# Optimization experiments

Measured on AMD Instinct MI355X. Metric: run time of the kernel, lower is better.

## Reference

```python
import jax, jax.numpy as jnp
import numpy as np

N_NODES = 50000
N_EDGES = 800000
D = 64
N_BASIS = 8


def setup_inputs() -> dict:
    key = jax.random.key(0)
    ks = jax.random.split(key, 16)
    inp = {
        "p": jax.random.normal(ks[0], (N_NODES, D), dtype=jnp.float32),
        "idx_i": jax.random.randint(ks[1], (N_EDGES,), 0, N_NODES),
        "idx_j": jax.random.randint(ks[2], (N_EDGES,), 0, N_NODES),
        "basis": jax.random.normal(ks[3], (N_EDGES, N_BASIS), dtype=jnp.float32),
        # pp_layer MLP: [64, 64, 64], activation tanh between layers
        "pp_W1": jax.random.normal(ks[4], (D, D), dtype=jnp.float32) / np.sqrt(D),
        "pp_b1": jnp.zeros((D,), dtype=jnp.float32),
        "pp_W2": jax.random.normal(ks[5], (D, D), dtype=jnp.float32) / np.sqrt(D),
        "pp_b2": jnp.zeros((D,), dtype=jnp.float32),
        # pi_layer MLP: n_neurons = [128, 64, 64, 64*8], activation=None, last layer no bias
        "pi_W1": jax.random.normal(ks[6], (2 * D, D), dtype=jnp.float32) / np.sqrt(2 * D),
        "pi_b1": jnp.zeros((D,), dtype=jnp.float32),
        "pi_W2": jax.random.normal(ks[7], (D, D), dtype=jnp.float32) / np.sqrt(D),
        "pi_b2": jnp.zeros((D,), dtype=jnp.float32),
        "pi_W3": jax.random.normal(ks[8], (D, D * N_BASIS), dtype=jnp.float32) / np.sqrt(D),
        # ii_layer MLP: [64, 64, 64], activation tanh between layers
        "ii_W1": jax.random.normal(ks[9], (D, D), dtype=jnp.float32) / np.sqrt(D),
        "ii_b1": jnp.zeros((D,), dtype=jnp.float32),
        "ii_W2": jax.random.normal(ks[10], (D, D), dtype=jnp.float32) / np.sqrt(D),
        "ii_b2": jnp.zeros((D,), dtype=jnp.float32),
    }
    return inp


def reference(p, idx_i, idx_j, basis,
              pp_W1, pp_b1, pp_W2, pp_b2,
              pi_W1, pi_b1, pi_W2, pi_b2, pi_W3,
              ii_W1, ii_b1, ii_W2, ii_b2):
    # pp_layer: node MLP (tanh between layers, no activation after last)
    p1 = jnp.tanh(p @ pp_W1 + pp_b1) @ pp_W2 + pp_b2          # [N, D]

    # PILayer: gather endpoint features, concat, linear MLP (activation=None), basis contraction
    inter = jnp.concatenate([p1[idx_i], p1[idx_j]], axis=-1)  # [E, 2D]
    inter = inter @ pi_W1 + pi_b1                              # [E, D]
    inter = inter @ pi_W2 + pi_b2                              # [E, D]
    inter = inter @ pi_W3                                      # [E, D*n_basis] (no bias)
    inter = inter.reshape(inter.shape[0], D, N_BASIS)          # [E, D, n_basis]
    i1 = jnp.einsum('ecb,eb->ec', inter, basis)                # [E, D]

    # ii_layer: edge MLP
    i1 = jnp.tanh(i1 @ ii_W1 + ii_b1) @ ii_W2 + ii_b2          # [E, D]

    # IPLayer: scatter_add edge features back to nodes (dim_size = p1.shape[0])
    out = jax.ops.segment_sum(i1, idx_j, num_segments=p1.shape[0])  # [N, D]
    return out
```

## Files before the change

### kernel.cpp

```cpp
#include <hip/hip_runtime.h>

#define N_NODES 50000
#define N_EDGES 800000
#define NPAD 50176

typedef float f32x4 __attribute__((ext_vector_type(4)));
typedef short bf16x8 __attribute__((ext_vector_type(8)));

__device__ __forceinline__ float fast_tanh(float x) {
  float e = __expf(2.0f * x);
  float r;
  asm("v_rcp_f32 %0, %1" : "=v"(r) : "v"(e + 1.0f));
  return fmaf(-2.0f, r, 1.0f);
}

__device__ __forceinline__ unsigned short f2bf_rne(float x) {
  unsigned u = __float_as_uint(x);
  unsigned r = u + 0x7FFFu + ((u >> 16) & 1u);
  return (unsigned short)(r >> 16);
}

__device__ __forceinline__ void gemm8(const float* __restrict__ sXrow,
                                      const float* __restrict__ sW,
                                      int lane, float acc[8]) {
  for (int k = 0; k < 64; k += 4) {
    float w0 = sW[k * 64 + lane];
    float w1 = sW[(k + 1) * 64 + lane];
    float w2 = sW[(k + 2) * 64 + lane];
    float w3 = sW[(k + 3) * 64 + lane];
    #pragma unroll
    for (int r = 0; r < 8; ++r) {
      float4 x = *(const float4*)(sXrow + r * 64 + k);
      acc[r] = fmaf(x.x, w0, fmaf(x.y, w1, fmaf(x.z, w2, fmaf(x.w, w3, acc[r]))));
    }
  }
}

__global__ __launch_bounds__(256) void front_kernel(
    const float* __restrict__ p, const int* __restrict__ idx_j,
    const float* __restrict__ ppW1, const float* __restrict__ ppb1,
    const float* __restrict__ ppW2, const float* __restrict__ ppb2,
    const float* __restrict__ piW1, const float* __restrict__ pib1,
    const float* __restrict__ piW2, const float* __restrict__ pib2,
    const float* __restrict__ piW3, const float* __restrict__ iiW1,
    const float* __restrict__ iiW2,
    int* __restrict__ counts,
    float* __restrict__ qa, float* __restrict__ qb, float* __restrict__ b12,
    unsigned short* __restrict__ Bpack, unsigned short* __restrict__ W2pack) {
  int bid = blockIdx.x;
  int tid = threadIdx.x;

  if (bid >= 1708) {
    int e = (bid - 1708) * 256 + tid;
    if (e < N_EDGES) atomicAdd(&counts[idx_j[e]], 1);
    return;
  }
  if (bid >= 1563) {
    int gid = (bid - 1563) * 256 + tid;
    if (gid < 32768) {
      int j = gid & 7;
      int lane = (gid >> 3) & 63;
      int ct = (gid >> 9) & 3;
      int ks = gid >> 11;
      int kidx = ks * 32 + ((lane >> 4) << 3) + j;
      int col = ct * 16 + (lane & 15);
      int k = kidx >> 3, b = kidx & 7;
      float acc = 0.f;
      #pragma unroll 8
      for (int mm = 0; mm < 64; ++mm)
        acc = fmaf(piW3[k * 512 + mm * 8 + b], iiW1[mm * 64 + col], acc);
      Bpack[gid] = f2bf_rne(acc);
    } else if (gid < 32832) {
      int c = gid - 32768;
      float acc = pib2[c];
      for (int k = 0; k < 64; ++k) acc = fmaf(pib1[k], piW2[k * 64 + c], acc);
      b12[c] = acc;
    } else if (gid < 36928) {
      int g2 = gid - 32832;
      int j = g2 & 7;
      int lane = (g2 >> 3) & 63;
      int ct = (g2 >> 9) & 3;
      int ks = g2 >> 11;
      int kidx = ks * 32 + ((lane >> 4) << 3) + j;
      int col = ct * 16 + (lane & 15);
      W2pack[g2] = f2bf_rne(iiW2[kidx * 64 + col]);
    }
    return;
  }

  __shared__ float sW[64 * 64];
  __shared__ float sX[4][8][64];
  __shared__ float sY[4][8][64];
  int wave = tid >> 6, lane = tid & 63;
  int rowbase = bid * 32 + wave * 8;

  float4* sXf4 = (float4*)&sX[wave][0][0];
  for (int t = lane; t < 128; t += 64) {
    int r = t >> 4, c4 = t & 15;
    int row = rowbase + r;
    float4 v = make_float4(0.f, 0.f, 0.f, 0.f);
    if (row < N_NODES) v = ((const float4*)p)[row * 16 + c4];
    sXf4[t] = v;
  }
  for (int i = tid; i < 4096; i += 256) sW[i] = ppW1[i];
  __syncthreads();
  float h[8];
  {
    float bv = ppb1[lane];
    #pragma unroll
    for (int r = 0; r < 8; ++r) h[r] = bv;
  }
  gemm8(&sX[wave][0][0], sW, lane, h);
  #pragma unroll
  for (int r = 0; r < 8; ++r) sY[wave][r][lane] = fast_tanh(h[r]);
  __syncthreads();
  for (int i = tid; i < 4096; i += 256) sW[i] = ppW2[i];
  __syncthreads();
  float g[8];
  {
    float bv = ppb2[lane];
    #pragma unroll
    for (int r = 0; r < 8; ++r) g[r] = bv;
  }
  gemm8(&sY[wave][0][0], sW, lane, g);
  #pragma unroll
  for (int r = 0; r < 8; ++r) sX[wave][r][lane] = g[r];
  __syncthreads();
  for (int i = tid; i < 4096; i += 256) sW[i] = piW1[i];
  __syncthreads();
  float t1[8] = {0, 0, 0, 0, 0, 0, 0, 0};
  gemm8(&sX[wave][0][0], sW, lane, t1);
  #pragma unroll
  for (int r = 0; r < 8; ++r) sY[wave][r][lane] = t1[r];
  __syncthreads();
  for (int i = tid; i < 4096; i += 256) sW[i] = piW1[4096 + i];
  __syncthreads();
  float t2[8] = {0, 0, 0, 0, 0, 0, 0, 0};
  gemm8(&sX[wave][0][0], sW, lane, t2);
  __syncthreads();
  #pragma unroll
  for (int r = 0; r < 8; ++r) sX[wave][r][lane] = t2[r];
  __syncthreads();
  for (int i = tid; i < 4096; i += 256) sW[i] = piW2[i];
  __syncthreads();
  float a[8] = {0, 0, 0, 0, 0, 0, 0, 0};
  float b[8] = {0, 0, 0, 0, 0, 0, 0, 0};
  for (int k = 0; k < 64; k += 4) {
    float w0 = sW[k * 64 + lane];
    float w1 = sW[(k + 1) * 64 + lane];
    float w2 = sW[(k + 2) * 64 + lane];
    float w3 = sW[(k + 3) * 64 + lane];
    #pragma unroll
    for (int r = 0; r < 8; ++r) {
      float4 x = *(const float4*)(&sY[wave][r][k]);
      float4 y = *(const float4*)(&sX[wave][r][k]);
      a[r] = fmaf(x.x, w0, fmaf(x.y, w1, fmaf(x.z, w2, fmaf(x.w, w3, a[r]))));
      b[r] = fmaf(y.x, w0, fmaf(y.y, w1, fmaf(y.z, w2, fmaf(y.w, w3, b[r]))));
    }
  }
  #pragma unroll
  for (int r = 0; r < 8; ++r) {
    int row = rowbase + r;
    if (row < N_NODES) {
      qa[row * 64 + lane] = a[r];
      qb[row * 64 + lane] = b[r];
    }
  }
}

__global__ __launch_bounds__(1024) void scan_kernel(
    const int* __restrict__ counts, int* __restrict__ cursors) {
  __shared__ int buf[1024];
  __shared__ int red[16];
  int b = blockIdx.x, tid = threadIdx.x;
  int idx = b * 1024 + tid;
  int v = counts[idx];
  buf[tid] = v;
  int partial = 0;
  for (int i = tid; i < b * 1024; i += 1024) partial += counts[i];
  #pragma unroll
  for (int off = 32; off >= 1; off >>= 1) partial += __shfl_down(partial, off, 64);
  if ((tid & 63) == 0) red[tid >> 6] = partial;
  __syncthreads();
  for (int off = 1; off < 1024; off <<= 1) {
    int t = (tid >= off) ? buf[tid - off] : 0;
    __syncthreads();
    buf[tid] += t;
    __syncthreads();
  }
  int base = 0;
  #pragma unroll
  for (int i = 0; i < 16; ++i) base += red[i];
  cursors[idx] = base + buf[tid] - v;
}

__global__ __launch_bounds__(256) void sort_scatter_kernel(
    const int* __restrict__ idx_i, const int* __restrict__ idx_j,
    int* __restrict__ cursors,
    int2* __restrict__ sorted_ij, int* __restrict__ sorted_e) {
  int e = blockIdx.x * 256 + threadIdx.x;
  if (e < N_EDGES) {
    int j = idx_j[e];
    int pos = atomicAdd(&cursors[j], 1);
    sorted_ij[pos] = make_int2(idx_i[e], j);
    sorted_e[pos] = e;
  }
}

__global__ __launch_bounds__(1024, 8) void edge_kernel(
    const int2* __restrict__ sorted_ij, const int* __restrict__ sorted_e,
    const float* __restrict__ basis,
    const float* __restrict__ qa, const float* __restrict__ qb,
    const float* __restrict__ b12,
    const unsigned short* __restrict__ Bpack,
    const unsigned short* __restrict__ W2pack,
    const float* __restrict__ iib1, const float* __restrict__ iib2,
    float* __restrict__ out) {
  __shared__ __align__(16) unsigned short sB[32768];
  float* sH2 = (float*)sB;
  unsigned short* sT = sB;
  float* sF = (float*)sB;

  int tid = threadIdx.x;
  int e0 = blockIdx.x * 256;

  for (int t = tid; t < 4096; t += 1024) {
    int e = t >> 4, q = t & 15;
    int2 se = sorted_ij[e0 + e];
    float4 va = ((const float4*)qa)[se.x * 16 + q];
    float4 vb = ((const float4*)qb)[se.y * 16 + q];
    float4 vc = ((const float4*)b12)[q];
    float4 h;
    h.x = va.x + vb.x + vc.x;
    h.y = va.y + vb.y + vc.y;
    h.z = va.z + vb.z + vc.z;
    h.w = va.w + vb.w + vc.w;
    int dw = e * 64 + ((q * 4) ^ ((e & 7) << 3));
    *((float4*)(sH2 + dw)) = h;
  }
  __syncthreads();

  int w = tid >> 6, l = tid & 63;
  int m = l & 15, s = l >> 4;
  int eloc = w * 16 + m;
  int swz = (eloc & 7) << 3;

  float h2r[16];
  #pragma unroll
  for (int t = 0; t < 16; ++t) h2r[t] = sH2[eloc * 64 + ((t * 4 + s) ^ swz)];

  float bas[8];
  {
    int eorig = sorted_e[e0 + eloc];
    const float4* bp = (const float4*)(basis + (size_t)eorig * 8);
    float4 b0 = bp[0], b1 = bp[1];
    bas[0] = b0.x; bas[1] = b0.y; bas[2] = b0.z; bas[3] = b0.w;
    bas[4] = b1.x; bas[5] = b1.y; bas[6] = b1.z; bas[7] = b1.w;
  }
  __syncthreads();

  {
    const uint4* g = (const uint4*)Bpack;
    uint4* d = (uint4*)sB;
    #pragma unroll
    for (int t = 0; t < 4; ++t) d[tid + t * 1024] = g[tid + t * 1024];
  }
  __syncthreads();

  f32x4 c0, c1, c2, c3;
  {
    float v0 = iib1[m], v1 = iib1[16 + m], v2 = iib1[32 + m], v3 = iib1[48 + m];
    c0 = (f32x4){v0, v0, v0, v0};
    c1 = (f32x4){v1, v1, v1, v1};
    c2 = (f32x4){v2, v2, v2, v2};
    c3 = (f32x4){v3, v3, v3, v3};
  }

  const bf16x8* Bl = (const bf16x8*)sB;
  #pragma unroll
  for (int ks = 0; ks < 16; ++ks) {
    bf16x8 B0 = Bl[(ks * 4 + 0) * 64 + l];
    bf16x8 B1 = Bl[(ks * 4 + 1) * 64 + l];
    bf16x8 B2 = Bl[(ks * 4 + 2) * 64 + l];
    bf16x8 B3 = Bl[(ks * 4 + 3) * 64 + l];
    float hv = h2r[ks];
    union { unsigned u[4]; bf16x8 v; } A;
    #pragma unroll
    for (int j = 0; j < 4; ++j) {
      float p0 = hv * bas[2 * j];
      float p1 = hv * bas[2 * j + 1];
      asm("v_cvt_pk_bf16_f32 %0, %1, %2" : "=v"(A.u[j]) : "v"(p0), "v"(p1));
    }
    c0 = __builtin_amdgcn_mfma_f32_16x16x32_bf16(A.v, B0, c0, 0, 0, 0);
    c1 = __builtin_amdgcn_mfma_f32_16x16x32_bf16(A.v, B1, c1, 0, 0, 0);
    c2 = __builtin_amdgcn_mfma_f32_16x16x32_bf16(A.v, B2, c2, 0, 0, 0);
    c3 = __builtin_amdgcn_mfma_f32_16x16x32_bf16(A.v, B3, c3, 0, 0, 0);
  }
  __syncthreads();

  #pragma unroll
  for (int r = 0; r < 4; ++r) {
    int row = w * 16 + s * 4 + r;
    sT[row * 72 + 0 * 16 + m] = f2bf_rne(fast_tanh(c0[r]));
    sT[row * 72 + 1 * 16 + m] = f2bf_rne(fast_tanh(c1[r]));
    sT[row * 72 + 2 * 16 + m] = f2bf_rne(fast_tanh(c2[r]));
    sT[row * 72 + 3 * 16 + m] = f2bf_rne(fast_tanh(c3[r]));
  }
  __syncthreads();

  f32x4 d0, d1, d2, d3;
  {
    float v0 = iib2[m], v1 = iib2[16 + m], v2 = iib2[32 + m], v3 = iib2[48 + m];
    d0 = (f32x4){v0, v0, v0, v0};
    d1 = (f32x4){v1, v1, v1, v1};
    d2 = (f32x4){v2, v2, v2, v2};
    d3 = (f32x4){v3, v3, v3, v3};
  }
  const bf16x8* Wl = (const bf16x8*)W2pack;
  #pragma unroll
  for (int ks = 0; ks < 2; ++ks) {
    bf16x8 Af = *(const bf16x8*)(sT + eloc * 72 + ks * 32 + s * 8);
    d0 = __builtin_amdgcn_mfma_f32_16x16x32_bf16(Af, Wl[(ks * 4 + 0) * 64 + l], d0, 0, 0, 0);
    d1 = __builtin_amdgcn_mfma_f32_16x16x32_bf16(Af, Wl[(ks * 4 + 1) * 64 + l], d1, 0, 0, 0);
    d2 = __builtin_amdgcn_mfma_f32_16x16x32_bf16(Af, Wl[(ks * 4 + 2) * 64 + l], d2, 0, 0, 0);
    d3 = __builtin_amdgcn_mfma_f32_16x16x32_bf16(Af, Wl[(ks * 4 + 3) * 64 + l], d3, 0, 0, 0);
  }

  #pragma unroll
  for (int h = 0; h < 2; ++h) {
    __syncthreads();
    if ((w >> 3) == h) {
      int wl = w & 7;
      #pragma unroll
      for (int r = 0; r < 4; ++r) {
        int row = wl * 16 + s * 4 + r;
        sF[row * 68 + 0  + m] = d0[r];
        sF[row * 68 + 16 + m] = d1[r];
        sF[row * 68 + 32 + m] = d2[r];
        sF[row * 68 + 48 + m] = d3[r];
      }
    }
    __syncthreads();
    {
      int base_e = e0 + h * 128 + w * 8;
      float acc = sF[(w * 8) * 68 + l];
      int cur_j = sorted_ij[base_e].y;
      #pragma unroll
      for (int rr = 1; rr < 8; ++rr) {
        int nj = sorted_ij[base_e + rr].y;
        float v = sF[(w * 8 + rr) * 68 + l];
        if (nj == cur_j) {
          acc += v;
        } else {
          atomicAdd(&out[(size_t)cur_j * 64 + l], acc);
          acc = v;
          cur_j = nj;
        }
      }
      atomicAdd(&out[(size_t)cur_j * 64 + l], acc);
    }
  }
}

extern "C" void kernel_launch(void* const* d_in, const int* in_sizes, int n_in,
                              void* d_out, int out_size, void* d_ws, size_t ws_size,
                              hipStream_t stream) {
  const float* p     = (const float*)d_in[0];
  const int*   idx_i = (const int*)d_in[1];
  const int*   idx_j = (const int*)d_in[2];
  const float* basis = (const float*)d_in[3];
  const float* ppW1  = (const float*)d_in[4];
  const float* ppb1  = (const float*)d_in[5];
  const float* ppW2  = (const float*)d_in[6];
  const float* ppb2  = (const float*)d_in[7];
  const float* piW1  = (const float*)d_in[8];
  const float* pib1  = (const float*)d_in[9];
  const float* piW2  = (const float*)d_in[10];
  const float* pib2  = (const float*)d_in[11];
  const float* piW3  = (const float*)d_in[12];
  const float* iiW1  = (const float*)d_in[13];
  const float* iib1  = (const float*)d_in[14];
  const float* iiW2  = (const float*)d_in[15];
  const float* iib2  = (const float*)d_in[16];

  float* ws  = (float*)d_ws;
  float* qa  = ws;
  float* qb  = ws + 3200000;
  float* b12 = ws + 6400000;
  unsigned short* Bpack  = (unsigned short*)(ws + 6400064);
  unsigned short* W2pack = (unsigned short*)(ws + 6416448);
  int* counts    = (int*)(ws + 6418496);
  int* cursors   = (int*)(ws + 6468672);
  int2* sorted_ij = (int2*)(ws + 6518848);
  int* sorted_e   = (int*)(ws + 8118848);

  hipMemsetAsync(d_out, 0, (size_t)out_size * sizeof(float), stream);
  hipMemsetAsync(counts, 0, (size_t)NPAD * sizeof(int), stream);
  front_kernel<<<4833, 256, 0, stream>>>(p, idx_j, ppW1, ppb1, ppW2, ppb2,
                                         piW1, pib1, piW2, pib2, piW3, iiW1, iiW2,
                                         counts, qa, qb, b12, Bpack, W2pack);
  scan_kernel<<<49, 1024, 0, stream>>>(counts, cursors);
  sort_scatter_kernel<<<3125, 256, 0, stream>>>(idx_i, idx_j, cursors,
                                                sorted_ij, sorted_e);
  edge_kernel<<<3125, 1024, 0, stream>>>(sorted_ij, sorted_e, basis,
                                         qa, qb, b12, Bpack, W2pack,
                                         iib1, iib2, (float*)d_out);
}
```

Measured before the change: 300.6 us.

## Move node-side MLP chain in front kernel to bf16 MFMA with swizzled LDS

Rewrites the front kernel's node MLP chain (pp layers plus the pi_W1/pi_W2 projections) to use 16x16x32 bf16 MFMA instructions in place of scalar fp32 FMAs. Activations and weights are packed to bf16 in XOR-swizzled shared memory to avoid bank conflicts. Each block now handles 128 node rows with 512 threads, so the grid split for the counting and packing roles is rescaled. Intermediates are rounded to bf16, which costs accuracy in qa/qb, but this kernel is only one part of the total time.

```diff
diff --git a/kernel.cpp b/kernel.cpp
--- a/kernel.cpp
+++ b/kernel.cpp
@@ -20,23 +20,56 @@
   return (unsigned short)(r >> 16);
 }
 
-__device__ __forceinline__ void gemm8(const float* __restrict__ sXrow,
-                                      const float* __restrict__ sW,
-                                      int lane, float acc[8]) {
-  for (int k = 0; k < 64; k += 4) {
-    float w0 = sW[k * 64 + lane];
-    float w1 = sW[(k + 1) * 64 + lane];
-    float w2 = sW[(k + 2) * 64 + lane];
-    float w3 = sW[(k + 3) * 64 + lane];
-    #pragma unroll
-    for (int r = 0; r < 8; ++r) {
-      float4 x = *(const float4*)(sXrow + r * 64 + k);
-      acc[r] = fmaf(x.x, w0, fmaf(x.y, w1, fmaf(x.z, w2, fmaf(x.w, w3, acc[r]))));
-    }
-  }
-}
-
-__global__ __launch_bounds__(256) void front_kernel(
+__device__ __forceinline__ void packW(const float* __restrict__ W,
+                                      unsigned short* __restrict__ dst, int tid) {
+  int ks = tid >> 8, ct = (tid >> 6) & 3, lane = tid & 63;
+  int k0 = ks * 32 + ((lane >> 4) << 3);
+  int col = ct * 16 + (lane & 15);
+  const float* src = W + k0 * 64 + col;
+  unsigned u[4];
+  #pragma unroll
+  for (int jj = 0; jj < 4; ++jj) {
+    float v0 = src[(2 * jj) * 64];
+    float v1 = src[(2 * jj + 1) * 64];
+    asm("v_cvt_pk_bf16_f32 %0, %1, %2" : "=v"(u[jj]) : "v"(v0), "v"(v1));
+  }
+  *(uint4*)(dst + (size_t)tid * 8) = make_uint4(u[0], u[1], u[2], u[3]);
+}
+
+__device__ __forceinline__ void mfma_gemm(const unsigned short* __restrict__ actIn,
+                                          const unsigned short* __restrict__ bpk,
+                                          int w, int l, f32x4 acc[4]) {
+  int m = l & 15, s = l >> 4;
+  int row = w * 16 + m;
+  int sw = (m & 7) << 3;
+  #pragma unroll
+  for (int ks = 0; ks < 2; ++ks) {
+    bf16x8 a = *(const bf16x8*)(actIn + row * 64 + ((ks * 32 + s * 8) ^ sw));
+    #pragma unroll
+    for (int ct = 0; ct < 4; ++ct) {
+      bf16x8 b = *(const bf16x8*)(bpk + ((size_t)((ks * 4 + ct) * 64 + l)) * 8);
+      acc[ct] = __builtin_amdgcn_mfma_f32_16x16x32_bf16(a, b, acc[ct], 0, 0, 0);
+    }
+  }
+}
+
+__device__ __forceinline__ void store_act(unsigned short* __restrict__ actOut,
+                                          int w, int l, const f32x4 acc[4],
+                                          bool do_tanh) {
+  int m = l & 15, s = l >> 4;
+  #pragma unroll
+  for (int ct = 0; ct < 4; ++ct) {
+    #pragma unroll
+    for (int r = 0; r < 4; ++r) {
+      int row = w * 16 + s * 4 + r;
+      float v = acc[ct][r];
+      if (do_tanh) v = fast_tanh(v);
+      actOut[row * 64 + ((ct * 16 + m) ^ ((row & 7) << 3))] = f2bf_rne(v);
+    }
+  }
+}
+
+__global__ __launch_bounds__(512) void front_kernel(
     const float* __restrict__ p, const int* __restrict__ idx_j,
     const float* __restrict__ ppW1, const float* __restrict__ ppb1,
     const float* __restrict__ ppW2, const float* __restrict__ ppb2,
@@ -50,13 +83,13 @@
   int bid = blockIdx.x;
   int tid = threadIdx.x;
 
-  if (bid >= 1708) {
-    int e = (bid - 1708) * 256 + tid;
+  if (bid >= 464) {
+    int e = (bid - 464) * 512 + tid;
     if (e < N_EDGES) atomicAdd(&counts[idx_j[e]], 1);
     return;
   }
-  if (bid >= 1563) {
-    int gid = (bid - 1563) * 256 + tid;
+  if (bid >= 391) {
+    int gid = (bid - 391) * 512 + tid;
     if (gid < 32768) {
       int j = gid & 7;
       int lane = (gid >> 3) & 63;
@@ -88,83 +121,91 @@
     return;
   }
 
-  __shared__ float sW[64 * 64];
-  __shared__ float sX[4][8][64];
-  __shared__ float sY[4][8][64];
-  int wave = tid >> 6, lane = tid & 63;
-  int rowbase = bid * 32 + wave * 8;
-
-  float4* sXf4 = (float4*)&sX[wave][0][0];
-  for (int t = lane; t < 128; t += 64) {
-    int r = t >> 4, c4 = t & 15;
-    int row = rowbase + r;
+  __shared__ __align__(16) unsigned short sBpk[2][4096];
+  __shared__ __align__(16) unsigned short sAct[2][8192];
+
+  int w = tid >> 6, l = tid & 63;
+  int m = l & 15;
+  int nb0 = bid * 128;
+
+  for (int t = tid; t < 2048; t += 512) {
+    int row = t >> 4, q = t & 15;
+    int g = nb0 + row;
     float4 v = make_float4(0.f, 0.f, 0.f, 0.f);
-    if (row < N_NODES) v = ((const float4*)p)[row * 16 + c4];
-    sXf4[t] = v;
-  }
-  for (int i = tid; i < 4096; i += 256) sW[i] = ppW1[i];
-  __syncthreads();
-  float h[8];
-  {
-    float bv = ppb1[lane];
-    #pragma unroll
-    for (int r = 0; r < 8; ++r) h[r] = bv;
-  }
-  gemm8(&sX[wave][0][0], sW, lane, h);
-  #pragma unroll
-  for (int r = 0; r < 8; ++r) sY[wave][r][lane] = fast_tanh(h[r]);
-  __syncthreads();
-  for (int i = tid; i < 4096; i += 256) sW[i] = ppW2[i];
-  __syncthreads();
-  float g[8];
-  {
-    float bv = ppb2[lane];
-    #pragma unroll
-    for (int r = 0; r < 8; ++r) g[r] = bv;
-  }
-  gemm8(&sY[wave][0][0], sW, lane, g);
-  #pragma unroll
-  for (int r = 0; r < 8; ++r) sX[wave][r][lane] = g[r];
-  __syncthreads();
-  for (int i = tid; i < 4096; i += 256) sW[i] = piW1[i];
-  __syncthreads();
-  float t1[8] = {0, 0, 0, 0, 0, 0, 0, 0};
-  gemm8(&sX[wave][0][0], sW, lane, t1);
-  #pragma unroll
-  for (int r = 0; r < 8; ++r) sY[wave][r][lane] = t1[r];
-  __syncthreads();
-  for (int i = tid; i < 4096; i += 256) sW[i] = piW1[4096 + i];
-  __syncthreads();
-  float t2[8] = {0, 0, 0, 0, 0, 0, 0, 0};
-  gemm8(&sX[wave][0][0], sW, lane, t2);
-  __syncthreads();
-  #pragma unroll
-  for (int r = 0; r < 8; ++r) sX[wave][r][lane] = t2[r];
-  __syncthreads();
-  for (int i = tid; i < 4096; i += 256) sW[i] = piW2[i];
-  __syncthreads();
-  float a[8] = {0, 0, 0, 0, 0, 0, 0, 0};
-  float b[8] = {0, 0, 0, 0, 0, 0, 0, 0};
-  for (int k = 0; k < 64; k += 4) {
-    float w0 = sW[k * 64 + lane];
-    float w1 = sW[(k + 1) * 64 + lane];
-    float w2 = sW[(k + 2) * 64 + lane];
-    float w3 = sW[(k + 3) * 64 + lane];
-    #pragma unroll
-    for (int r = 0; r < 8; ++r) {
-      float4 x = *(const float4*)(&sY[wave][r][k]);
-      float4 y = *(const float4*)(&sX[wave][r][k]);
-      a[r] = fmaf(x.x, w0, fmaf(x.y, w1, fmaf(x.z, w2, fmaf(x.w, w3, a[r]))));
-      b[r] = fmaf(y.x, w0, fmaf(y.y, w1, fmaf(y.z, w2, fmaf(y.w, w3, b[r]))));
-    }
-  }
-  #pragma unroll
-  for (int r = 0; r < 8; ++r) {
-    int row = rowbase + r;
-    if (row < N_NODES) {
-      qa[row * 64 + lane] = a[r];
-      qb[row * 64 + lane] = b[r];
-    }
+    if (g < N_NODES) v = ((const float4*)p)[g * 16 + q];
+    unsigned u0, u1;
+    asm("v_cvt_pk_bf16_f32 %0, %1, %2" : "=v"(u0) : "v"(v.x), "v"(v.y));
+    asm("v_cvt_pk_bf16_f32 %0, %1, %2" : "=v"(u1) : "v"(v.z), "v"(v.w));
+    int sw = (row & 7) << 3;
+    *(uint2*)(&sAct[0][row * 64 + ((q * 4) ^ sw)]) = make_uint2(u0, u1);
+  }
+  packW(ppW1, sBpk[0], tid);
+  packW(ppW2, sBpk[1], tid);
+  __syncthreads();
+
+  f32x4 acc[4];
+  #pragma unroll
+  for (int ct = 0; ct < 4; ++ct) {
+    float bv = ppb1[ct * 16 + m];
+    acc[ct] = (f32x4){bv, bv, bv, bv};
+  }
+  mfma_gemm(sAct[0], sBpk[0], w, l, acc);
+  store_act(sAct[1], w, l, acc, true);
+  __syncthreads();
+
+  #pragma unroll
+  for (int ct = 0; ct < 4; ++ct) {
+    float bv = ppb2[ct * 16 + m];
+    acc[ct] = (f32x4){bv, bv, bv, bv};
+  }
+  mfma_gemm(sAct[1], sBpk[1], w, l, acc);
+  store_act(sAct[0], w, l, acc, false);
+  __syncthreads();
+
+  packW(piW1, sBpk[0], tid);
+  packW(piW2, sBpk[1], tid);
+  __syncthreads();
+
+  #pragma unroll
+  for (int ct = 0; ct < 4; ++ct) acc[ct] = (f32x4){0.f, 0.f, 0.f, 0.f};
+  mfma_gemm(sAct[0], sBpk[0], w, l, acc);
+  store_act(sAct[1], w, l, acc, false);
+  __syncthreads();
+
+  #pragma unroll
+  for (int ct = 0; ct < 4; ++ct) acc[ct] = (f32x4){0.f, 0.f, 0.f, 0.f};
+  mfma_gemm(sAct[1], sBpk[1], w, l, acc);
+  {
+    int s = l >> 4;
+    #pragma unroll
+    for (int ct = 0; ct < 4; ++ct)
+      #pragma unroll
+      for (int r = 0; r < 4; ++r) {
+        int rg = nb0 + w * 16 + s * 4 + r;
+        if (rg < N_NODES) qa[(size_t)rg * 64 + ct * 16 + m] = acc[ct][r];
+      }
+  }
+  packW(piW1 + 4096, sBpk[0], tid);
+  __syncthreads();
+
+  #pragma unroll
+  for (int ct = 0; ct < 4; ++ct) acc[ct] = (f32x4){0.f, 0.f, 0.f, 0.f};
+  mfma_gemm(sAct[0], sBpk[0], w, l, acc);
+  store_act(sAct[1], w, l, acc, false);
+  __syncthreads();
+
+  #pragma unroll
+  for (int ct = 0; ct < 4; ++ct) acc[ct] = (f32x4){0.f, 0.f, 0.f, 0.f};
+  mfma_gemm(sAct[1], sBpk[1], w, l, acc);
+  {
+    int s = l >> 4;
+    #pragma unroll
+    for (int ct = 0; ct < 4; ++ct)
+      #pragma unroll
+      for (int r = 0; r < 4; ++r) {
+        int rg = nb0 + w * 16 + s * 4 + r;
+        if (rg < N_NODES) qb[(size_t)rg * 64 + ct * 16 + m] = acc[ct][r];
+      }
   }
 }
 
@@ -396,7 +437,7 @@
 
   hipMemsetAsync(d_out, 0, (size_t)out_size * sizeof(float), stream);
   hipMemsetAsync(counts, 0, (size_t)NPAD * sizeof(int), stream);
-  front_kernel<<<4833, 256, 0, stream>>>(p, idx_j, ppW1, ppb1, ppW2, ppb2,
+  front_kernel<<<2027, 512, 0, stream>>>(p, idx_j, ppW1, ppb1, ppW2, ppb2,
                                          piW1, pib1, piW2, pib2, piW3, iiW1, iiW2,
                                          counts, qa, qb, b12, Bpack, W2pack);
   scan_kernel<<<49, 1024, 0, stream>>>(counts, cursors);
```

Result: faster. 252.0 us (-16.2%).
